# Optimization experiments

Measured on AMD Instinct MI355X. Metric: run time of the kernel, lower is better.

The kernel has to match this reference:

```python
import jax, jax.numpy as jnp
import numpy as np

B, S, D = 16, 1024, 768
H = 12
HD = D // H  # 64


def setup_inputs() -> dict:
    key = jax.random.key(0)
    ks = jax.random.split(key, 9)
    s = 1.0 / np.sqrt(D)
    x = jax.random.normal(ks[0], (B, S, D), dtype=jnp.float32)
    Wq = jax.random.uniform(ks[1], (H, HD, D), minval=-s, maxval=s, dtype=jnp.float32)
    bq = jax.random.uniform(ks[2], (H, HD), minval=-s, maxval=s, dtype=jnp.float32)
    Wk = jax.random.uniform(ks[3], (H, HD, D), minval=-s, maxval=s, dtype=jnp.float32)
    bk = jax.random.uniform(ks[4], (H, HD), minval=-s, maxval=s, dtype=jnp.float32)
    Wv = jax.random.uniform(ks[5], (H, HD, D), minval=-s, maxval=s, dtype=jnp.float32)
    bv = jax.random.uniform(ks[6], (H, HD), minval=-s, maxval=s, dtype=jnp.float32)
    Wo = jax.random.uniform(ks[7], (D, D), minval=-s, maxval=s, dtype=jnp.float32)
    bo = jax.random.uniform(ks[8], (D,), minval=-s, maxval=s, dtype=jnp.float32)
    return {"x": x, "Wq": Wq, "bq": bq, "Wk": Wk, "bk": bk,
            "Wv": Wv, "bv": bv, "Wo": Wo, "bo": bo}


def reference(x, Wq, bq, Wk, bk, Wv, bv, Wo, bo):
    # per-head projections: [B,S,D] x [H,HD,D] -> [B,H,S,HD]
    q = jnp.einsum('bsd,hed->bhse', x, Wq) + bq[None, :, None, :]
    k = jnp.einsum('bsd,hed->bhse', x, Wk) + bk[None, :, None, :]
    v = jnp.einsum('bsd,hed->bhse', x, Wv) + bv[None, :, None, :]
    scores = jnp.einsum('bhse,bhte->bhst', q, k) / jnp.sqrt(jnp.float32(HD))
    weights = jax.nn.softmax(scores, axis=-1)  # [B,H,S,S]
    attn = jnp.einsum('bhst,bhte->bhse', weights, v)  # [B,H,S,HD]
    # concat heads along last dim (head order matches torch.cat)
    concat = attn.transpose(0, 2, 1, 3).reshape(B, S, H * HD)
    out = concat @ Wo.T + bo
    return out
```

## Files before the change

kernel.cpp:

```cpp
#include <hip/hip_runtime.h>
#include <hip/hip_bf16.h>

typedef unsigned short u16;
typedef unsigned int u32;
typedef __attribute__((ext_vector_type(2))) unsigned int u32x2;
typedef __attribute__((ext_vector_type(4))) unsigned int u32x4;
typedef __attribute__((ext_vector_type(4))) float f32x4;
typedef __attribute__((ext_vector_type(16))) float f32x16;
typedef __attribute__((ext_vector_type(8))) short s16x8;
typedef __attribute__((ext_vector_type(4))) unsigned short u16x4;
typedef __attribute__((ext_vector_type(8))) unsigned short u16x8;

#define QSCALE 0.18033688011112042f

#define BARRIER() do { __builtin_amdgcn_s_barrier(); __builtin_amdgcn_sched_barrier(0); } while (0)
#define WAIT_VM0() do { asm volatile("s_waitcnt vmcnt(0)" ::: "memory"); __builtin_amdgcn_sched_barrier(0); } while (0)

__device__ inline u16 f2bf(float f) {
  union { float f; unsigned u; } x; x.f = f;
  unsigned r = x.u + 0x7FFFu + ((x.u >> 16) & 1u);
  return (u16)(r >> 16);
}

__device__ inline u32 cvtpk(float lo, float hi) {
  u32 r;
  asm("v_cvt_pk_bf16_f32 %0, %1, %2" : "=v"(r) : "v"(lo), "v"(hi));
  return r;
}

__device__ inline void pl32swap(u32& a, u32& b) {
  asm("v_permlane32_swap_b32 %0, %1" : "+v"(a), "+v"(b));
}

__global__ void cvt_all(const float* __restrict__ x,
                        const float* __restrict__ Wq, const float* __restrict__ Wk,
                        const float* __restrict__ Wv, const float* __restrict__ Wo,
                        const float* __restrict__ bq, const float* __restrict__ bk,
                        const float* __restrict__ bv,
                        u16* __restrict__ xb, u16* __restrict__ wqkv,
                        u16* __restrict__ wo, float* __restrict__ bqkv) {
  int i = blockIdx.x * blockDim.x + threadIdx.x;
  const int NX = 3145728;
  const int NW = 147456;
  if (i < NX) {
    const float4 v = ((const float4*)x)[i];
    u16x4 o; o[0] = f2bf(v.x); o[1] = f2bf(v.y); o[2] = f2bf(v.z); o[3] = f2bf(v.w);
    ((u16x4*)xb)[i] = o;
    return;
  }
  i -= NX;
  if (i < 4 * NW) {
    const int w = i / NW, k = i - w * NW;
    const float* s = (w == 0) ? Wq : (w == 1) ? Wk : (w == 2) ? Wv : Wo;
    u16* d = (w == 3) ? wo : wqkv + (size_t)w * 589824;
    const float4 v = ((const float4*)s)[k];
    u16x4 o; o[0] = f2bf(v.x); o[1] = f2bf(v.y); o[2] = f2bf(v.z); o[3] = f2bf(v.w);
    ((u16x4*)d)[k] = o;
    return;
  }
  i -= 4 * NW;
  if (i < 576) {
    const int w = i / 192, k = i - w * 192;
    const float* s = (w == 0) ? bq : (w == 1) ? bk : bv;
    ((float4*)bqkv)[w * 192 + k] = ((const float4*)s)[k];
  }
}

template<int FC, int STORE_BF16, int QKV_SCALE>
__global__ __launch_bounds__(512, 2) void gemm8(
    const u16* __restrict__ A, const u16* __restrict__ Bm,
    const float* __restrict__ bias, void* __restrict__ C,
    int N, int K, int ntiles)
{
  constexpr int ASZ = 32768;
  constexpr int BSZ = FC * 8192;
  constexpr int BUF = ASZ + BSZ;
  __shared__ char lds[2 * BUF];

  const int tid = threadIdx.x, wave = tid >> 6, lane = tid & 63;
  const int il = lane & 15, g = lane >> 4;
  const int Lr = lane >> 3, Lc = lane & 7;
  const int wm = wave >> 2, wn = wave & 3;

  const int cpx = (int)gridDim.x >> 3;
  const int orig = (blockIdx.x & 7) * cpx + (blockIdx.x >> 3);
  const int tm = (orig / ntiles) * 256, tn = (orig % ntiles) * (FC * 64);

  const size_t Kb = (size_t)K * 2;
  const int colb = (Lc * 16) ^ (Lr << 4);

  auto stageAll = [&](int buf, int k0) {
    char* base = &lds[buf * BUF];
#pragma unroll
    for (int c = 0; c < 4; ++c) {
      const int row = tm + c * 64 + wave * 8 + Lr;
      const char* src = (const char*)A + (size_t)row * Kb + k0 * 2 + colb;
      __builtin_amdgcn_global_load_lds((const __attribute__((address_space(1))) void*)src,
          (__attribute__((address_space(3))) void*)(base + c * 8192 + wave * 1024), 16, 0, 0);
    }
#pragma unroll
    for (int c = 0; c < FC; ++c) {
      const int row = tn + c * 64 + wave * 8 + Lr;
      const char* src = (const char*)Bm + (size_t)row * Kb + k0 * 2 + colb;
      __builtin_amdgcn_global_load_lds((const __attribute__((address_space(1))) void*)src,
          (__attribute__((address_space(3))) void*)(base + ASZ + c * 8192 + wave * 1024), 16, 0, 0);
    }
  };
  auto ldA = [&](int buf, int fr, int kk) -> s16x8 {
    const int row = wm * 128 + fr * 16 + il;
    const int cb = (kk * 64 + g * 16) ^ ((il & 7) << 4);
    return *(const s16x8*)&lds[buf * BUF + row * 128 + cb];
  };
  auto ldB = [&](int buf, int fc, int kk) -> s16x8 {
    const int row = wn * (FC * 16) + fc * 16 + il;
    const int cb = (kk * 64 + g * 16) ^ ((il & 7) << 4);
    return *(const s16x8*)&lds[buf * BUF + ASZ + row * 128 + cb];
  };

  f32x4 acc[8][FC] = {};
  const int nK = K >> 6;

  stageAll(0, 0);
  WAIT_VM0();
  BARRIER();

  for (int t = 0; t < nK; ++t) {
    const int cur = t & 1;
    const bool pf = (t + 1 < nK);

    s16x8 bfr[FC][2];
#pragma unroll
    for (int fc = 0; fc < FC; ++fc) { bfr[fc][0] = ldB(cur, fc, 0); bfr[fc][1] = ldB(cur, fc, 1); }

#pragma unroll
    for (int p = 0; p < 4; ++p) {
      s16x8 a00 = ldA(cur, 2 * p, 0),     a01 = ldA(cur, 2 * p, 1);
      s16x8 a10 = ldA(cur, 2 * p + 1, 0), a11 = ldA(cur, 2 * p + 1, 1);
      if (p == 0 && pf) stageAll(cur ^ 1, (t + 1) << 6);
      BARRIER();
      __builtin_amdgcn_s_setprio(1);
#pragma unroll
      for (int fc = 0; fc < FC; ++fc) {
        acc[2*p][fc]   = __builtin_amdgcn_mfma_f32_16x16x32_bf16(a00, bfr[fc][0], acc[2*p][fc], 0, 0, 0);
        acc[2*p][fc]   = __builtin_amdgcn_mfma_f32_16x16x32_bf16(a01, bfr[fc][1], acc[2*p][fc], 0, 0, 0);
        acc[2*p+1][fc] = __builtin_amdgcn_mfma_f32_16x16x32_bf16(a10, bfr[fc][0], acc[2*p+1][fc], 0, 0, 0);
        acc[2*p+1][fc] = __builtin_amdgcn_mfma_f32_16x16x32_bf16(a11, bfr[fc][1], acc[2*p+1][fc], 0, 0, 0);
      }
      __builtin_amdgcn_s_setprio(0);
      if (p == 3 && pf) WAIT_VM0();
      BARRIER();
    }
  }

#pragma unroll
  for (int fr = 0; fr < 8; ++fr) {
    const int row0 = tm + wm * 128 + fr * 16 + g * 4;
#pragma unroll
    for (int fc = 0; fc < FC; ++fc) {
      const int col = tn + wn * (FC * 16) + fc * 16 + il;
      const float bb = bias[col];
#pragma unroll
      for (int r = 0; r < 4; ++r) {
        float v = acc[fr][fc][r] + bb;
        if (QKV_SCALE) { if (col < 768) v *= QSCALE; }
        if (STORE_BF16) ((u16*)C)[(size_t)(row0 + r) * N + col] = f2bf(v);
        else            ((float*)C)[(size_t)(row0 + r) * N + col] = v;
      }
    }
  }
}

__global__ __launch_bounds__(256) void transpose_v(const u16* __restrict__ qkv,
                                                   u16* __restrict__ vT) {
  __shared__ u16 T[64 * 64];
  const int kt = blockIdx.x, h = blockIdx.y, b = blockIdx.z;
  const int t = threadIdx.x;
  {
    const int k = t >> 2, c = (t & 3) * 16;
    const u16* src = qkv + (size_t)(b * 1024 + kt * 64 + k) * 2304 + 1536 + h * 64 + c;
    const int sw = ((k >> 3) & 7) << 4;
#pragma unroll
    for (int s2 = 0; s2 < 2; ++s2) {
      s16x8 v = *(const s16x8*)(src + s2 * 8);
      *(s16x8*)((char*)T + k * 128 + (((c + s2 * 8) * 2) ^ sw)) = v;
    }
  }
  __syncthreads();
  const int w = t >> 6, l = t & 63;
  const int kj = (l & 7) * 8;
  const int sw = (l & 7) << 4;
#pragma unroll
  for (int i = 0; i < 2; ++i) {
    const int e = w * 16 + i * 8 + (l >> 3);
    u16x8 o;
#pragma unroll
    for (int j = 0; j < 8; ++j)
      o[j] = *(const u16*)((const char*)T + (kj + j) * 128 + ((e * 2) ^ sw));
    *(u16x8*)(vT + ((size_t)(b * 12 + h) * 64 + e) * 1024 + kt * 64 + kj) = o;
  }
}

__global__ __launch_bounds__(256) void attn_fwd(const u16* __restrict__ qkv,
                                                const u16* __restrict__ vT,
                                                u16* __restrict__ concat)
{
  __shared__ u16 Kl[64 * 64];
  __shared__ u16 Vl[64 * 64];

  const int tid = threadIdx.x, wave = tid >> 6, lane = tid & 63;
  const int wg = blockIdx.x;
  const int bh = (wg & 7) | ((wg >> 6) << 3);
  const int qb = (wg >> 3) & 7;
  const int b = bh / 12, h = bh % 12;
  const int q = lane & 31, hi = lane >> 5;
  const int qs0 = qb * 128 + wave * 32;

  const char* qkvB = (const char*)qkv;
  const size_t rowB = (size_t)b * 1024 * 4608;
  const char* vtB = (const char*)vT + (size_t)bh * 64 * 2048;

  s16x8 qf[4];
  {
    const char* qp = qkvB + rowB + (size_t)(qs0 + q) * 4608 + h * 128 + hi * 16;
#pragma unroll
    for (int s = 0; s < 4; ++s) qf[s] = *(const s16x8*)(qp + s * 32);
  }

  float l_ = 0.f;
  f32x16 accO[2] = {};

  const int Lr = lane >> 3, Lc = lane & 7;
  const int colb = (Lc * 16) ^ ((Lr & 7) << 4);
  const int swk = (q & 7) << 4;

  for (int kv0 = 0; kv0 < 1024; kv0 += 64) {
#pragma unroll
    for (int i = 0; i < 2; ++i) {
      const int row = wave * 16 + i * 8 + Lr;
      const char* ks = qkvB + rowB + (size_t)(kv0 + row) * 4608 + 1536 + h * 128 + colb;
      __builtin_amdgcn_global_load_lds((const __attribute__((address_space(1))) void*)ks,
          (__attribute__((address_space(3))) void*)(Kl + (wave * 16 + i * 8) * 64), 16, 0, 0);
      const char* vs = vtB + (size_t)row * 2048 + kv0 * 2 + colb;
      __builtin_amdgcn_global_load_lds((const __attribute__((address_space(1))) void*)vs,
          (__attribute__((address_space(3))) void*)(Vl + (wave * 16 + i * 8) * 64), 16, 0, 0);
    }
    __syncthreads();

    f32x16 st[2] = {};
    __builtin_amdgcn_s_setprio(1);
#pragma unroll
    for (int s = 0; s < 4; ++s) {
      const int cb = (s * 32 + hi * 16) ^ swk;
      s16x8 k0 = *(const s16x8*)((const char*)Kl + q * 128 + cb);
      s16x8 k1 = *(const s16x8*)((const char*)Kl + (32 + q) * 128 + cb);
      st[0] = __builtin_amdgcn_mfma_f32_32x32x16_bf16(k0, qf[s], st[0], 0, 0, 0);
      st[1] = __builtin_amdgcn_mfma_f32_32x32x16_bf16(k1, qf[s], st[1], 0, 0, 0);
    }
    __builtin_amdgcn_s_setprio(0);

    float cs0 = 0.f, cs1 = 0.f;
#pragma unroll
    for (int r = 0; r < 16; ++r) {
      const float p0 = __builtin_amdgcn_exp2f(st[0][r]);
      const float p1 = __builtin_amdgcn_exp2f(st[1][r]);
      st[0][r] = p0; st[1][r] = p1;
      cs0 += p0; cs1 += p1;
    }
    l_ += cs0 + cs1;

    s16x8 pa[4];
#pragma unroll
    for (int kb = 0; kb < 2; ++kb)
#pragma unroll
      for (int ks = 0; ks < 2; ++ks) {
        u32 A0 = cvtpk(st[kb][ks * 8 + 0], st[kb][ks * 8 + 1]);
        u32 A1 = cvtpk(st[kb][ks * 8 + 2], st[kb][ks * 8 + 3]);
        u32 B0 = cvtpk(st[kb][ks * 8 + 4], st[kb][ks * 8 + 5]);
        u32 B1 = cvtpk(st[kb][ks * 8 + 6], st[kb][ks * 8 + 7]);
        pl32swap(A0, B0);
        pl32swap(A1, B1);
        u32x4 w = {A0, A1, B0, B1};
        pa[kb * 2 + ks] = __builtin_bit_cast(s16x8, w);
      }

    __builtin_amdgcn_s_setprio(1);
#pragma unroll
    for (int ksub = 0; ksub < 4; ++ksub) {
      const int cb = (ksub * 32 + hi * 16) ^ swk;
      s16x8 v0 = *(const s16x8*)((const char*)Vl + q * 128 + cb);
      s16x8 v1 = *(const s16x8*)((const char*)Vl + (32 + q) * 128 + cb);
      accO[0] = __builtin_amdgcn_mfma_f32_32x32x16_bf16(v0, pa[ksub], accO[0], 0, 0, 0);
      accO[1] = __builtin_amdgcn_mfma_f32_32x32x16_bf16(v1, pa[ksub], accO[1], 0, 0, 0);
    }
    __builtin_amdgcn_s_setprio(0);
    __syncthreads();
  }

  l_ += __shfl_xor(l_, 32);
  const float linv = __builtin_amdgcn_rcpf(l_);
  u16* crow = concat + ((size_t)b * 1024 + qs0 + q) * 768 + h * 64;
#pragma unroll
  for (int eb = 0; eb < 2; ++eb)
#pragma unroll
    for (int rq = 0; rq < 4; ++rq) {
      u32 w0 = cvtpk(accO[eb][rq * 4 + 0] * linv, accO[eb][rq * 4 + 1] * linv);
      u32 w1 = cvtpk(accO[eb][rq * 4 + 2] * linv, accO[eb][rq * 4 + 3] * linv);
      u32x2 w = {w0, w1};
      *(u16x4*)(crow + eb * 32 + rq * 8 + hi * 4) = __builtin_bit_cast(u16x4, w);
    }
}

extern "C" void kernel_launch(void* const* d_in, const int* in_sizes, int n_in,
                              void* d_out, int out_size, void* d_ws, size_t ws_size,
                              hipStream_t stream) {
  const float* x  = (const float*)d_in[0];
  const float* Wq = (const float*)d_in[1];
  const float* bq = (const float*)d_in[2];
  const float* Wk = (const float*)d_in[3];
  const float* bk = (const float*)d_in[4];
  const float* Wv = (const float*)d_in[5];
  const float* bv = (const float*)d_in[6];
  const float* Wo = (const float*)d_in[7];
  const float* bo = (const float*)d_in[8];

  const size_t XN = (size_t)16384 * 768;
  const size_t WN = (size_t)768 * 768;

  u16* xb   = (u16*)d_ws;
  u16* wqkv = xb + XN;
  u16* wo   = wqkv + 3 * WN;
  float* bqkv = (float*)(wo + WN);
  u16* qkv  = (u16*)(bqkv + 2304);
  u16* vt   = qkv + (size_t)16384 * 2304;
  u16* cc   = xb;

  cvt_all<<<(3736128 + 255) / 256, 256, 0, stream>>>(
      x, Wq, Wk, Wv, Wo, bq, bk, bv, xb, wqkv, wo, bqkv);

  gemm8<3, 1, 1><<<768, 512, 0, stream>>>(xb, wqkv, bqkv, qkv, 2304, 768, 12);

  transpose_v<<<dim3(16, 12, 16), 256, 0, stream>>>(qkv, vt);

  attn_fwd<<<1536, 256, 0, stream>>>(qkv, vt, cc);

  gemm8<3, 0, 0><<<256, 512, 0, stream>>>(cc, wo, bo, d_out, 768, 768, 4);
}
```

Measured before the change: 191.8 us.

## Software-pipeline attention K/V loads via registers with 128-wide KV tiles

Restructures the attention kernel so each workgroup handles 256 queries in two chunks, and the grid is halved. KV tiles are widened to 128 rows, and the next tile is prefetched into registers while the current one is computed, then written to swizzled LDS. This replaces the direct global-to-LDS loads that ran with no overlap. It also adds an XCD-aware block remap. The costs are more registers, extra barriers, and fewer workgroups, which may reduce occupancy.

```diff
diff --git a/kernel.cpp b/kernel.cpp
--- a/kernel.cpp
+++ b/kernel.cpp
@@ -204,110 +204,151 @@
                                                 const u16* __restrict__ vT,
                                                 u16* __restrict__ concat)
 {
-  __shared__ u16 Kl[64 * 64];
-  __shared__ u16 Vl[64 * 64];
+  __shared__ u16 Kl[128 * 64];
+  __shared__ u16 Vt[64 * 128];
 
   const int tid = threadIdx.x, wave = tid >> 6, lane = tid & 63;
   const int wg = blockIdx.x;
-  const int bh = (wg & 7) | ((wg >> 6) << 3);
-  const int qb = (wg >> 3) & 7;
+  const int orig = (wg & 7) * 96 + (wg >> 3);
+  const int bh = orig >> 2, qsuper = orig & 3;
   const int b = bh / 12, h = bh % 12;
   const int q = lane & 31, hi = lane >> 5;
-  const int qs0 = qb * 128 + wave * 32;
-
-  const char* qkvB = (const char*)qkv;
-  const size_t rowB = (size_t)b * 1024 * 4608;
-  const char* vtB = (const char*)vT + (size_t)bh * 64 * 2048;
-
-  s16x8 qf[4];
-  {
-    const char* qp = qkvB + rowB + (size_t)(qs0 + q) * 4608 + h * 128 + hi * 16;
-#pragma unroll
-    for (int s = 0; s < 4; ++s) qf[s] = *(const s16x8*)(qp + s * 32);
-  }
-
-  float l_ = 0.f;
-  f32x16 accO[2] = {};
-
   const int Lr = lane >> 3, Lc = lane & 7;
-  const int colb = (Lc * 16) ^ ((Lr & 7) << 4);
+
+  const char* qkvB = (const char*)qkv + (size_t)b * 1024 * 4608;
+  const char* vtB  = (const char*)vT + (size_t)bh * 64 * 2048;
+  char* KlB = (char*)Kl;
+  char* VtB = (char*)Vt;
+
   const int swk = (q & 7) << 4;
-
-  for (int kv0 = 0; kv0 < 1024; kv0 += 64) {
-#pragma unroll
-    for (int i = 0; i < 2; ++i) {
-      const int row = wave * 16 + i * 8 + Lr;
-      const char* ks = qkvB + rowB + (size_t)(kv0 + row) * 4608 + 1536 + h * 128 + colb;
-      __builtin_amdgcn_global_load_lds((const __attribute__((address_space(1))) void*)ks,
-          (__attribute__((address_space(3))) void*)(Kl + (wave * 16 + i * 8) * 64), 16, 0, 0);
-      const char* vs = vtB + (size_t)row * 2048 + kv0 * 2 + colb;
-      __builtin_amdgcn_global_load_lds((const __attribute__((address_space(1))) void*)vs,
-          (__attribute__((address_space(3))) void*)(Vl + (wave * 16 + i * 8) * 64), 16, 0, 0);
+  const int swv = (q & 15) << 4;
+
+  const int krow0 = wave * 32 + Lr;
+  const int kcol  = Lc * 16;
+  const int erow0 = wave * 16 + (lane >> 4);
+  const int vcol  = (lane & 15) * 16;
+
+  int kwoff[4], vwoff[4];
+#pragma unroll
+  for (int i = 0; i < 4; ++i) {
+    const int kr = krow0 + i * 8;
+    kwoff[i] = kr * 128 + (kcol ^ ((kr & 7) << 4));
+    const int er = erow0 + i * 4;
+    vwoff[i] = er * 256 + (vcol ^ ((er & 15) << 4));
+  }
+
+  for (int chunk = 0; chunk < 2; ++chunk) {
+    const int qs0 = qsuper * 256 + chunk * 128 + wave * 32;
+
+    s16x8 qf[4];
+    {
+      const char* qp = qkvB + (size_t)(qs0 + q) * 4608 + h * 128 + hi * 16;
+#pragma unroll
+      for (int s = 0; s < 4; ++s) qf[s] = *(const s16x8*)(qp + s * 32);
+    }
+
+    float l_ = 0.f;
+    f32x16 accO[2] = {};
+
+    u32x4 kreg[4], vreg[4];
+#pragma unroll
+    for (int i = 0; i < 4; ++i) {
+      kreg[i] = *(const u32x4*)(qkvB + (size_t)(krow0 + i * 8) * 4608 + 1536 + h * 128 + kcol);
+      vreg[i] = *(const u32x4*)(vtB + (size_t)(erow0 + i * 4) * 2048 + vcol);
+    }
+#pragma unroll
+    for (int i = 0; i < 4; ++i) {
+      *(u32x4*)(KlB + kwoff[i]) = kreg[i];
+      *(u32x4*)(VtB + vwoff[i]) = vreg[i];
     }
     __syncthreads();
 
-    f32x16 st[2] = {};
-    __builtin_amdgcn_s_setprio(1);
-#pragma unroll
-    for (int s = 0; s < 4; ++s) {
-      const int cb = (s * 32 + hi * 16) ^ swk;
-      s16x8 k0 = *(const s16x8*)((const char*)Kl + q * 128 + cb);
-      s16x8 k1 = *(const s16x8*)((const char*)Kl + (32 + q) * 128 + cb);
-      st[0] = __builtin_amdgcn_mfma_f32_32x32x16_bf16(k0, qf[s], st[0], 0, 0, 0);
-      st[1] = __builtin_amdgcn_mfma_f32_32x32x16_bf16(k1, qf[s], st[1], 0, 0, 0);
-    }
-    __builtin_amdgcn_s_setprio(0);
-
-    float cs0 = 0.f, cs1 = 0.f;
-#pragma unroll
-    for (int r = 0; r < 16; ++r) {
-      const float p0 = __builtin_amdgcn_exp2f(st[0][r]);
-      const float p1 = __builtin_amdgcn_exp2f(st[1][r]);
-      st[0][r] = p0; st[1][r] = p1;
-      cs0 += p0; cs1 += p1;
-    }
-    l_ += cs0 + cs1;
-
-    s16x8 pa[4];
-#pragma unroll
-    for (int kb = 0; kb < 2; ++kb)
-#pragma unroll
-      for (int ks = 0; ks < 2; ++ks) {
-        u32 A0 = cvtpk(st[kb][ks * 8 + 0], st[kb][ks * 8 + 1]);
-        u32 A1 = cvtpk(st[kb][ks * 8 + 2], st[kb][ks * 8 + 3]);
-        u32 B0 = cvtpk(st[kb][ks * 8 + 4], st[kb][ks * 8 + 5]);
-        u32 B1 = cvtpk(st[kb][ks * 8 + 6], st[kb][ks * 8 + 7]);
-        pl32swap(A0, B0);
-        pl32swap(A1, B1);
-        u32x4 w = {A0, A1, B0, B1};
-        pa[kb * 2 + ks] = __builtin_bit_cast(s16x8, w);
-      }
-
-    __builtin_amdgcn_s_setprio(1);
-#pragma unroll
-    for (int ksub = 0; ksub < 4; ++ksub) {
-      const int cb = (ksub * 32 + hi * 16) ^ swk;
-      s16x8 v0 = *(const s16x8*)((const char*)Vl + q * 128 + cb);
-      s16x8 v1 = *(const s16x8*)((const char*)Vl + (32 + q) * 128 + cb);
-      accO[0] = __builtin_amdgcn_mfma_f32_32x32x16_bf16(v0, pa[ksub], accO[0], 0, 0, 0);
-      accO[1] = __builtin_amdgcn_mfma_f32_32x32x16_bf16(v1, pa[ksub], accO[1], 0, 0, 0);
-    }
-    __builtin_amdgcn_s_setprio(0);
-    __syncthreads();
-  }
-
-  l_ += __shfl_xor(l_, 32);
-  const float linv = __builtin_amdgcn_rcpf(l_);
-  u16* crow = concat + ((size_t)b * 1024 + qs0 + q) * 768 + h * 64;
-#pragma unroll
-  for (int eb = 0; eb < 2; ++eb)
-#pragma unroll
-    for (int rq = 0; rq < 4; ++rq) {
-      u32 w0 = cvtpk(accO[eb][rq * 4 + 0] * linv, accO[eb][rq * 4 + 1] * linv);
-      u32 w1 = cvtpk(accO[eb][rq * 4 + 2] * linv, accO[eb][rq * 4 + 3] * linv);
-      u32x2 w = {w0, w1};
-      *(u16x4*)(crow + eb * 32 + rq * 8 + hi * 4) = __builtin_bit_cast(u16x4, w);
-    }
+    for (int t = 0; t < 8; ++t) {
+      if (t < 7) {
+        const int kv0 = (t + 1) << 7;
+#pragma unroll
+        for (int i = 0; i < 4; ++i) {
+          kreg[i] = *(const u32x4*)(qkvB + (size_t)(kv0 + krow0 + i * 8) * 4608 + 1536 + h * 128 + kcol);
+          vreg[i] = *(const u32x4*)(vtB + (size_t)(erow0 + i * 4) * 2048 + kv0 * 2 + vcol);
+        }
+        __builtin_amdgcn_sched_barrier(0);
+      }
+
+#pragma unroll
+      for (int half = 0; half < 2; ++half) {
+        f32x16 st[2] = {};
+        __builtin_amdgcn_s_setprio(1);
+#pragma unroll
+        for (int s = 0; s < 4; ++s) {
+          const int cb = (s * 32 + hi * 16) ^ swk;
+          s16x8 k0 = *(const s16x8*)(KlB + (half * 64 + q) * 128 + cb);
+          s16x8 k1 = *(const s16x8*)(KlB + (half * 64 + 32 + q) * 128 + cb);
+          st[0] = __builtin_amdgcn_mfma_f32_32x32x16_bf16(k0, qf[s], st[0], 0, 0, 0);
+          st[1] = __builtin_amdgcn_mfma_f32_32x32x16_bf16(k1, qf[s], st[1], 0, 0, 0);
+        }
+        __builtin_amdgcn_s_setprio(0);
+
+        float cs0 = 0.f, cs1 = 0.f;
+#pragma unroll
+        for (int r = 0; r < 16; ++r) {
+          const float p0 = __builtin_amdgcn_exp2f(st[0][r]);
+          const float p1 = __builtin_amdgcn_exp2f(st[1][r]);
+          st[0][r] = p0; st[1][r] = p1;
+          cs0 += p0; cs1 += p1;
+        }
+        l_ += cs0 + cs1;
+
+        s16x8 pa[4];
+#pragma unroll
+        for (int kb = 0; kb < 2; ++kb)
+#pragma unroll
+          for (int ks = 0; ks < 2; ++ks) {
+            u32 A0 = cvtpk(st[kb][ks * 8 + 0], st[kb][ks * 8 + 1]);
+            u32 A1 = cvtpk(st[kb][ks * 8 + 2], st[kb][ks * 8 + 3]);
+            u32 B0 = cvtpk(st[kb][ks * 8 + 4], st[kb][ks * 8 + 5]);
+            u32 B1 = cvtpk(st[kb][ks * 8 + 6], st[kb][ks * 8 + 7]);
+            pl32swap(A0, B0);
+            pl32swap(A1, B1);
+            u32x4 w = {A0, A1, B0, B1};
+            pa[kb * 2 + ks] = __builtin_bit_cast(s16x8, w);
+          }
+
+        __builtin_amdgcn_s_setprio(1);
+#pragma unroll
+        for (int ksub = 0; ksub < 4; ++ksub) {
+          const int cb = (half * 128 + ksub * 32 + hi * 16) ^ swv;
+          s16x8 v0 = *(const s16x8*)(VtB + q * 256 + cb);
+          s16x8 v1 = *(const s16x8*)(VtB + (32 + q) * 256 + cb);
+          accO[0] = __builtin_amdgcn_mfma_f32_32x32x16_bf16(v0, pa[ksub], accO[0], 0, 0, 0);
+          accO[1] = __builtin_amdgcn_mfma_f32_32x32x16_bf16(v1, pa[ksub], accO[1], 0, 0, 0);
+        }
+        __builtin_amdgcn_s_setprio(0);
+      }
+
+      __syncthreads();
+      if (t < 7) {
+#pragma unroll
+        for (int i = 0; i < 4; ++i) {
+          *(u32x4*)(KlB + kwoff[i]) = kreg[i];
+          *(u32x4*)(VtB + vwoff[i]) = vreg[i];
+        }
+        __syncthreads();
+      }
+    }
+
+    l_ += __shfl_xor(l_, 32);
+    const float linv = __builtin_amdgcn_rcpf(l_);
+    u16* crow = concat + ((size_t)b * 1024 + qs0 + q) * 768 + h * 64;
+#pragma unroll
+    for (int eb = 0; eb < 2; ++eb)
+#pragma unroll
+      for (int rq = 0; rq < 4; ++rq) {
+        u32 w0 = cvtpk(accO[eb][rq * 4 + 0] * linv, accO[eb][rq * 4 + 1] * linv);
+        u32 w1 = cvtpk(accO[eb][rq * 4 + 2] * linv, accO[eb][rq * 4 + 3] * linv);
+        u32x2 w = {w0, w1};
+        *(u16x4*)(crow + eb * 32 + rq * 8 + hi * 4) = __builtin_bit_cast(u16x4, w);
+      }
+  }
 }
 
 extern "C" void kernel_launch(void* const* d_in, const int* in_sizes, int n_in,
@@ -341,7 +382,7 @@
 
   transpose_v<<<dim3(16, 12, 16), 256, 0, stream>>>(qkv, vt);
 
-  attn_fwd<<<1536, 256, 0, stream>>>(qkv, vt, cc);
+  attn_fwd<<<768, 256, 0, stream>>>(qkv, vt, cc);
 
   gemm8<3, 0, 0><<<256, 512, 0, stream>>>(cc, wo, bo, d_out, 768, 768, 4);
 }
```

Result: slower. 227.5 us (+18.6%).

## Fuse V transpose into QKV GEMM epilogue and double-buffer attention K/V tiles

Applied to the files above, without the earlier changes.

The QKV GEMM epilogue now writes the V columns straight into the transposed vT layout, which removes the separate transpose_v kernel and its extra read and write of V. The attention kernel now uses 512-thread blocks covering 256 queries, with double-buffered K/V LDS tiles, so the next tile's global-to-LDS load overlaps the current tile's compute. A new block-to-tile remap changes which blocks run together. The risks are that the epilogue's transposed stores are strided 8-byte writes, and the loop now has only one sync per iteration for the double buffer, which looks hazardous.

```diff
diff --git a/kernel.cpp b/kernel.cpp
--- a/kernel.cpp
+++ b/kernel.cpp
@@ -66,10 +66,11 @@
   }
 }
 
-template<int FC, int STORE_BF16, int QKV_SCALE>
+template<int FC, int STORE_BF16, int QKV_SCALE, int WV>
 __global__ __launch_bounds__(512, 2) void gemm8(
     const u16* __restrict__ A, const u16* __restrict__ Bm,
     const float* __restrict__ bias, void* __restrict__ C,
+    u16* __restrict__ vt,
     int N, int K, int ntiles)
 {
   constexpr int ASZ = 32768;
@@ -152,6 +153,23 @@
     }
   }
 
+  if (WV && tn >= 1536) {
+#pragma unroll
+    for (int fr = 0; fr < 8; ++fr) {
+      const int row0 = tm + wm * 128 + fr * 16 + g * 4;
+      const int bb_ = row0 >> 10, s0 = row0 & 1023;
+#pragma unroll
+      for (int fc = 0; fc < FC; ++fc) {
+        const int hcol = tn + wn * (FC * 16) + fc * 16 + il - 1536;
+        const float bb = bias[hcol + 1536];
+        u16x4 o;
+#pragma unroll
+        for (int r = 0; r < 4; ++r) o[r] = f2bf(acc[fr][fc][r] + bb);
+        *(u16x4*)(vt + ((size_t)(bb_ * 12 + (hcol >> 6)) * 64 + (hcol & 63)) * 1024 + s0) = o;
+      }
+    }
+    return;
+  }
 #pragma unroll
   for (int fr = 0; fr < 8; ++fr) {
     const int row0 = tm + wm * 128 + fr * 16 + g * 4;
@@ -170,58 +188,27 @@
   }
 }
 
-__global__ __launch_bounds__(256) void transpose_v(const u16* __restrict__ qkv,
-                                                   u16* __restrict__ vT) {
-  __shared__ u16 T[64 * 64];
-  const int kt = blockIdx.x, h = blockIdx.y, b = blockIdx.z;
-  const int t = threadIdx.x;
-  {
-    const int k = t >> 2, c = (t & 3) * 16;
-    const u16* src = qkv + (size_t)(b * 1024 + kt * 64 + k) * 2304 + 1536 + h * 64 + c;
-    const int sw = ((k >> 3) & 7) << 4;
-#pragma unroll
-    for (int s2 = 0; s2 < 2; ++s2) {
-      s16x8 v = *(const s16x8*)(src + s2 * 8);
-      *(s16x8*)((char*)T + k * 128 + (((c + s2 * 8) * 2) ^ sw)) = v;
-    }
-  }
-  __syncthreads();
-  const int w = t >> 6, l = t & 63;
-  const int kj = (l & 7) * 8;
-  const int sw = (l & 7) << 4;
-#pragma unroll
-  for (int i = 0; i < 2; ++i) {
-    const int e = w * 16 + i * 8 + (l >> 3);
-    u16x8 o;
-#pragma unroll
-    for (int j = 0; j < 8; ++j)
-      o[j] = *(const u16*)((const char*)T + (kj + j) * 128 + ((e * 2) ^ sw));
-    *(u16x8*)(vT + ((size_t)(b * 12 + h) * 64 + e) * 1024 + kt * 64 + kj) = o;
-  }
-}
-
-__global__ __launch_bounds__(256) void attn_fwd(const u16* __restrict__ qkv,
-                                                const u16* __restrict__ vT,
-                                                u16* __restrict__ concat)
+__global__ __launch_bounds__(512, 6) void attn_fwd(const u16* __restrict__ qkv,
+                                                   const u16* __restrict__ vT,
+                                                   u16* __restrict__ concat)
 {
-  __shared__ u16 Kl[64 * 64];
-  __shared__ u16 Vl[64 * 64];
+  __shared__ u16 Kl[2][64 * 64];
+  __shared__ u16 Vl[2][64 * 64];
 
   const int tid = threadIdx.x, wave = tid >> 6, lane = tid & 63;
   const int wg = blockIdx.x;
-  const int bh = (wg & 7) | ((wg >> 6) << 3);
-  const int qb = (wg >> 3) & 7;
+  const int orig = (wg & 7) * 96 + (wg >> 3);
+  const int bh = orig >> 2, qb = orig & 3;
   const int b = bh / 12, h = bh % 12;
   const int q = lane & 31, hi = lane >> 5;
-  const int qs0 = qb * 128 + wave * 32;
-
-  const char* qkvB = (const char*)qkv;
-  const size_t rowB = (size_t)b * 1024 * 4608;
-  const char* vtB = (const char*)vT + (size_t)bh * 64 * 2048;
+  const int qs0 = qb * 256 + wave * 32;
+
+  const char* qkvB = (const char*)qkv + (size_t)b * 1024 * 4608;
+  const char* vtB  = (const char*)vT + (size_t)bh * 64 * 2048;
 
   s16x8 qf[4];
   {
-    const char* qp = qkvB + rowB + (size_t)(qs0 + q) * 4608 + h * 128 + hi * 16;
+    const char* qp = qkvB + (size_t)(qs0 + q) * 4608 + h * 128 + hi * 16;
 #pragma unroll
     for (int s = 0; s < 4; ++s) qf[s] = *(const s16x8*)(qp + s * 32);
   }
@@ -230,29 +217,34 @@
   f32x16 accO[2] = {};
 
   const int Lr = lane >> 3, Lc = lane & 7;
-  const int colb = (Lc * 16) ^ ((Lr & 7) << 4);
+  const int colb = (Lc * 16) ^ (Lr << 4);
   const int swk = (q & 7) << 4;
 
-  for (int kv0 = 0; kv0 < 1024; kv0 += 64) {
-#pragma unroll
-    for (int i = 0; i < 2; ++i) {
-      const int row = wave * 16 + i * 8 + Lr;
-      const char* ks = qkvB + rowB + (size_t)(kv0 + row) * 4608 + 1536 + h * 128 + colb;
-      __builtin_amdgcn_global_load_lds((const __attribute__((address_space(1))) void*)ks,
-          (__attribute__((address_space(3))) void*)(Kl + (wave * 16 + i * 8) * 64), 16, 0, 0);
-      const char* vs = vtB + (size_t)row * 2048 + kv0 * 2 + colb;
-      __builtin_amdgcn_global_load_lds((const __attribute__((address_space(1))) void*)vs,
-          (__attribute__((address_space(3))) void*)(Vl + (wave * 16 + i * 8) * 64), 16, 0, 0);
-    }
-    __syncthreads();
+  auto stage = [&](int buf, int kv0) {
+    const int row = wave * 8 + Lr;
+    const char* ks = qkvB + (size_t)(kv0 + row) * 4608 + 1536 + h * 128 + colb;
+    __builtin_amdgcn_global_load_lds((const __attribute__((address_space(1))) void*)ks,
+        (__attribute__((address_space(3))) void*)(&Kl[buf][wave * 512]), 16, 0, 0);
+    const char* vs = vtB + (size_t)row * 2048 + kv0 * 2 + colb;
+    __builtin_amdgcn_global_load_lds((const __attribute__((address_space(1))) void*)vs,
+        (__attribute__((address_space(3))) void*)(&Vl[buf][wave * 512]), 16, 0, 0);
+  };
+
+  stage(0, 0);
+  __syncthreads();
+
+  for (int t = 0; t < 16; ++t) {
+    const int cur = t & 1;
+    if (t < 15) stage(cur ^ 1, (t + 1) << 6);
+    __builtin_amdgcn_sched_barrier(0);
 
     f32x16 st[2] = {};
     __builtin_amdgcn_s_setprio(1);
 #pragma unroll
     for (int s = 0; s < 4; ++s) {
       const int cb = (s * 32 + hi * 16) ^ swk;
-      s16x8 k0 = *(const s16x8*)((const char*)Kl + q * 128 + cb);
-      s16x8 k1 = *(const s16x8*)((const char*)Kl + (32 + q) * 128 + cb);
+      s16x8 k0 = *(const s16x8*)((const char*)&Kl[cur][0] + q * 128 + cb);
+      s16x8 k1 = *(const s16x8*)((const char*)&Kl[cur][0] + (32 + q) * 128 + cb);
       st[0] = __builtin_amdgcn_mfma_f32_32x32x16_bf16(k0, qf[s], st[0], 0, 0, 0);
       st[1] = __builtin_amdgcn_mfma_f32_32x32x16_bf16(k1, qf[s], st[1], 0, 0, 0);
     }
@@ -287,8 +279,8 @@
 #pragma unroll
     for (int ksub = 0; ksub < 4; ++ksub) {
       const int cb = (ksub * 32 + hi * 16) ^ swk;
-      s16x8 v0 = *(const s16x8*)((const char*)Vl + q * 128 + cb);
-      s16x8 v1 = *(const s16x8*)((const char*)Vl + (32 + q) * 128 + cb);
+      s16x8 v0 = *(const s16x8*)((const char*)&Vl[cur][0] + q * 128 + cb);
+      s16x8 v1 = *(const s16x8*)((const char*)&Vl[cur][0] + (32 + q) * 128 + cb);
       accO[0] = __builtin_amdgcn_mfma_f32_32x32x16_bf16(v0, pa[ksub], accO[0], 0, 0, 0);
       accO[1] = __builtin_amdgcn_mfma_f32_32x32x16_bf16(v1, pa[ksub], accO[1], 0, 0, 0);
     }
@@ -337,11 +329,9 @@
   cvt_all<<<(3736128 + 255) / 256, 256, 0, stream>>>(
       x, Wq, Wk, Wv, Wo, bq, bk, bv, xb, wqkv, wo, bqkv);
 
-  gemm8<3, 1, 1><<<768, 512, 0, stream>>>(xb, wqkv, bqkv, qkv, 2304, 768, 12);
-
-  transpose_v<<<dim3(16, 12, 16), 256, 0, stream>>>(qkv, vt);
-
-  attn_fwd<<<1536, 256, 0, stream>>>(qkv, vt, cc);
-
-  gemm8<3, 0, 0><<<256, 512, 0, stream>>>(cc, wo, bo, d_out, 768, 768, 4);
-}
+  gemm8<3, 1, 1, 1><<<768, 512, 0, stream>>>(xb, wqkv, bqkv, qkv, vt, 2304, 768, 12);
+
+  attn_fwd<<<768, 512, 0, stream>>>(qkv, vt, cc);
+
+  gemm8<3, 0, 0, 0><<<256, 512, 0, stream>>>(cc, wo, bo, d_out, nullptr, 768, 768, 4);
+}
```

New measurement: 243.0 us. 26.7% more time.
